# Kernel tuning notes

Measured on AMD Instinct MI355X. Metric: run time of the kernel, lower is better.

Reference implementation:

```python
import jax, jax.numpy as jnp
import numpy as np
from math import pi

B, L, S, D, H, M, DK, IND, KS = 8, 3072, 3072, 512, 8, 2, 64, 96, 25


def _linear(x, W, b):
    return x @ W + b


def _moving_avg(x, k):
    # Autoformer-style moving average with edge replication, stride 1.  x: [B, T, D]
    pad = (k - 1) // 2
    xp = jnp.concatenate([jnp.repeat(x[:, :1], pad, axis=1), x,
                          jnp.repeat(x[:, -1:], pad, axis=1)], axis=1)
    c = jnp.cumsum(xp, axis=1)
    c = jnp.concatenate([jnp.zeros_like(c[:, :1]), c], axis=1)
    return (c[:, k:] - c[:, :-k]) / k


def _trend_norm(x, g, b):
    # series_decomp(kernel=25): LayerNorm the seasonal part, add back the trend.
    trend = _moving_avg(x, KS)
    seas = x - trend
    mu = jnp.mean(seas, axis=-1, keepdims=True)
    var = jnp.var(seas, axis=-1, keepdims=True)
    return (seas - mu) * jax.lax.rsqrt(var + 1e-5) * g + b + trend


def _quat_attention(q, k, v, q_om, q_th, k_om, k_th):
    # q: [B,Lq,H,E]; k,v: [B,Sk,H,E]; omegas/thetas: [B,*,H,M]
    Bq, Lq, Hh, E = q.shape
    Sk = k.shape[1]
    Mm = q_om.shape[-1]
    qpos = (jnp.arange(Lq, dtype=q.dtype) / Lq)[None, :, None, None]
    kpos = (jnp.arange(Sk, dtype=q.dtype) / Sk)[None, :, None, None]
    Qa = q_om * qpos + q_th
    Ka = k_om * kpos + k_th
    Qc, Qs = jnp.cos(Qa), jnp.sin(Qa)
    Kc, Ks = jnp.cos(Ka), jnp.sin(Ka)
    q0, q1, q2, q3 = jnp.split(q, 4, axis=-1)
    k0, k1, k2, k3 = jnp.split(k, 4, axis=-1)
    op = lambda a, t: jnp.einsum('blhe,blhm->blhme', a, t)
    Qr = jnp.concatenate([op(q0, Qc) - op(q1, Qs), op(q1, Qc) + op(q0, Qs),
                          op(q2, Qc) + op(q3, Qs), op(q3, Qc) - op(q2, Qs)], axis=-1)
    Kr = jnp.concatenate([op(k0, Kc) - op(k2, Ks), op(k1, Kc) - op(k3, Ks),
                          op(k2, Kc) + op(k0, Ks), op(k3, Kc) + op(k1, Ks)], axis=-1)
    scores = jnp.einsum('blhme,bshme->bhls', Qr, Kr) / Mm
    scale = 1.0 / jnp.sqrt(jnp.asarray(E, q.dtype))
    A = jax.nn.softmax(scale * scores, axis=-1)
    return jnp.einsum('bhls,bshd->blhd', A, v)


def _ltr_layer(p, queries, keys, values):
    Bq, Lq, _ = queries.shape
    Sk = keys.shape[1]
    # kernel_size=1 convs == pointwise linears
    q_om = jax.nn.relu(_linear(queries, p['Wqo'], p['bqo'])).reshape(Bq, Lq, H, M)
    k_om = jax.nn.relu(_linear(keys, p['Wko'], p['bko'])).reshape(Bq, Sk, H, M)
    q_th = (jnp.tanh(_linear(queries, p['Wqt'], p['bqt'])) * pi).reshape(Bq, Lq, H, M)
    k_th = (jnp.tanh(_linear(keys, p['Wkt'], p['bkt'])) * pi).reshape(Bq, Sk, H, M)
    q = _linear(queries, p['Wq'], p['bq']).reshape(Bq, Lq, H, DK)
    k = _linear(keys, p['Wk'], p['bk']).reshape(Bq, Sk, H, DK)
    v = _linear(values, p['Wv'], p['bv']).reshape(Bq, Sk, H, DK)
    out = _quat_attention(q, k, v, q_om, q_th, k_om, k_th).reshape(Bq, Lq, H * DK)
    # D-matrix penalty == first-order difference along sequence
    om_pen = jnp.sum(jnp.diff(q_om, axis=1) ** 2) + jnp.sum(jnp.diff(k_om, axis=1) ** 2)
    th_pen = jnp.sum(q_th ** 2) + jnp.sum(k_th ** 2)
    return _linear(out, p['Wo'], p['bo']), om_pen, th_pen


def setup_inputs() -> dict:
    key = jax.random.key(0)
    ks = iter(jax.random.split(key, 32))
    rn = lambda shape, s=1.0: jax.random.normal(next(ks), shape, jnp.float32) * s
    w = 0.03  # ~1/sqrt(d_model)
    return dict(
        queries=rn((B, L, D)), keys=rn((B, S, D)), values=rn((B, S, D)),
        Wq=rn((2, D, D), w), bq=jnp.zeros((2, D), jnp.float32),
        Wk=rn((2, D, D), w), bk=jnp.zeros((2, D), jnp.float32),
        Wv=rn((2, D, D), w), bv=jnp.zeros((2, D), jnp.float32),
        Wqo=rn((2, D, M * H), w), bqo=jnp.zeros((2, M * H), jnp.float32),
        Wko=rn((2, D, M * H), w), bko=jnp.zeros((2, M * H), jnp.float32),
        Wqt=rn((2, D, M * H), w), bqt=jnp.zeros((2, M * H), jnp.float32),
        Wkt=rn((2, D, M * H), w), bkt=jnp.zeros((2, M * H), jnp.float32),
        Wo=rn((2, D, D), w), bo=jnp.zeros((2, D), jnp.float32),
        I=rn((1, IND, D), w),
        ln_g=jnp.ones((D,), jnp.float32), ln_b=jnp.zeros((D,), jnp.float32),
    )


def reference(queries, keys, values, Wq, bq, Wk, bk, Wv, bv, Wqo, bqo, Wko, bko,
              Wqt, bqt, Wkt, bkt, Wo, bo, I, ln_g, ln_b):
    def lp(i):
        return dict(Wq=Wq[i], bq=bq[i], Wk=Wk[i], bk=bk[i], Wv=Wv[i], bv=bv[i],
                    Wqo=Wqo[i], bqo=bqo[i], Wko=Wko[i], bko=bko[i],
                    Wqt=Wqt[i], bqt=bqt[i], Wkt=Wkt[i], bkt=bkt[i],
                    Wo=Wo[i], bo=bo[i])
    Bq = queries.shape[0]
    inducings = jnp.broadcast_to(I, (Bq, IND, D))
    inducings, om1, th1 = _ltr_layer(lp(0), inducings, keys, values)
    inducings = _trend_norm(inducings, ln_g, ln_b)
    out, om2, th2 = _ltr_layer(lp(1), queries, inducings, inducings)
    return out, om1 + om2, th1 + th2
```

## Files before the change

### kernel.cpp

```cpp
#include <hip/hip_runtime.h>
#include <math.h>

#define PI_F 3.14159265358979323846f

namespace {
constexpr int B_ = 8;
constexpr int L_ = 3072;
constexpr int S_ = 3072;
constexpr int H_ = 8;
constexpr int NF = 544;
constexpr int NSC = 8;
constexpr int SCHUNK = S_ / NSC;
}

typedef __attribute__((ext_vector_type(8))) short bf16x8;
typedef __attribute__((ext_vector_type(4))) float f32x4;

__device__ inline f32x4 mfma16(bf16x8 a, bf16x8 b, f32x4 c) {
  return __builtin_amdgcn_mfma_f32_16x16x32_bf16(a, b, c, 0, 0, 0);
}

__device__ inline ushort f2bf(float f) {
  union { float f; unsigned u; } v;
  v.f = f;
  unsigned r = v.u + 0x7FFFu + ((v.u >> 16) & 1u);
  return (ushort)(r >> 16);
}

__device__ inline void gl_lds16(const void* g, void* l) {
  __builtin_amdgcn_global_load_lds(
      (const __attribute__((address_space(1))) unsigned int*)g,
      (__attribute__((address_space(3))) unsigned int*)l, 16, 0, 0);
}

__device__ inline int xcd_swizzle(int flat, int nwg) {
  int q = nwg >> 3, r = nwg & 7;
  int xcd = flat & 7, ix = flat >> 3;
  return (xcd < r ? xcd * (q + 1) : r * (q + 1) + (xcd - r) * q) + ix;
}

__global__ void init_pen(float* pen) {
  if (threadIdx.x < 16) pen[threadIdx.x] = 0.f;
}

__global__ void write_pen(const float* __restrict__ pen, float* __restrict__ out) {
  if (threadIdx.x == 0) out[12582912] = pen[0];
  if (threadIdx.x == 1) out[12582913] = pen[1];
}

__global__ void pack_w(const float* __restrict__ Wm, const float* __restrict__ Wo_,
                       const float* __restrict__ Wt, const float* __restrict__ bm,
                       const float* __restrict__ bo_, const float* __restrict__ bt,
                       float* __restrict__ Wcat, float* __restrict__ bcat) {
  int gid = blockIdx.x * 256 + threadIdx.x;
  if (gid < 512 * 544) {
    int k = gid / 544, n = gid % 544;
    float v;
    if (n < 512) v = Wm[(size_t)k * 512 + n];
    else if (n < 528) v = Wo_[k * 16 + (n - 512)];
    else v = Wt[k * 16 + (n - 528)];
    Wcat[gid] = v;
  }
  if (gid < 544) {
    float v;
    if (gid < 512) v = bm[gid];
    else if (gid < 528) v = bo_[gid - 512];
    else v = bt[gid - 528];
    bcat[gid] = v;
  }
}

__global__ void pack_wt_fused(const float* __restrict__ Wm, const float* __restrict__ Wo_,
                              const float* __restrict__ Wt, const float* __restrict__ bm,
                              const float* __restrict__ bo_, const float* __restrict__ bt,
                              ushort* __restrict__ BT, float* __restrict__ bias) {
  int gid = blockIdx.x * 256 + threadIdx.x;
  if (gid < 640 * 512) {
    int n = gid >> 9, k = gid & 511;
    float v = 0.f;
    if (n < 512) v = Wm[(size_t)k * 512 + n];
    else if (n < 528) v = Wo_[k * 16 + (n - 512)];
    else if (n < 544) v = Wt[k * 16 + (n - 528)];
    BT[gid] = f2bf(v);
  }
  if (gid < 544)
    bias[gid] = (gid < 512) ? bm[gid] : (gid < 528 ? bo_[gid - 512] : bt[gid - 528]);
}

__global__ void pack_wt_plain(const float* __restrict__ W, const float* __restrict__ b,
                              ushort* __restrict__ BT, float* __restrict__ bias) {
  int gid = blockIdx.x * 256 + threadIdx.x;
  if (gid < 512 * 512) {
    int n = gid >> 9, k = gid & 511;
    BT[gid] = f2bf(W[(size_t)k * 512 + n]);
  }
  if (gid < 512) bias[gid] = b[gid];
}

__global__ __launch_bounds__(256)
void cast_bf16(const float* __restrict__ src, ushort* __restrict__ dst, int n8) {
  int gid = blockIdx.x * 256 + threadIdx.x;
  if (gid < n8) {
    float4 a = ((const float4*)src)[(size_t)gid * 2];
    float4 b = ((const float4*)src)[(size_t)gid * 2 + 1];
    ushort u[8] = {f2bf(a.x), f2bf(a.y), f2bf(a.z), f2bf(a.w),
                   f2bf(b.x), f2bf(b.y), f2bf(b.z), f2bf(b.w)};
    ((uint4*)dst)[gid] = *(uint4*)u;
  }
}

__global__ __launch_bounds__(256)
void gemm_bf16_mfma(const ushort* __restrict__ A, const ushort* __restrict__ BT,
                    const float* __restrict__ bias, void* __restrict__ Cv,
                    int ldc, int Nout, int act, int obf) {
  __shared__ ushort As[2][128][32];
  __shared__ ushort Bs[2][128][32];
  const int tid = threadIdx.x;
  const int wv = tid >> 6, lane = tid & 63, quad = lane >> 4, col = lane & 15;
  const int wm = wv & 1, wn = wv >> 1;

  const int nwg = gridDim.x * gridDim.y;
  const int flat = blockIdx.y * gridDim.x + blockIdx.x;
  const int nf = xcd_swizzle(flat, nwg);
  const int bx = nf % gridDim.x, by = nf / gridDim.x;
  const int m0 = by * 128, n0 = bx * 128;

  const int srow = lane >> 2;
  const int scol = (lane & 3) * 8;

  f32x4 acc[4][4];
#pragma unroll
  for (int i = 0; i < 4; ++i)
#pragma unroll
    for (int j = 0; j < 4; ++j) {
      f32x4 z = {0.f, 0.f, 0.f, 0.f};
      acc[i][j] = z;
    }

  const ushort* Ag = A + (size_t)(m0 + wv * 32) * 512;
  const ushort* Bg = BT + (size_t)(n0 + wv * 32) * 512;

  auto stage = [&](int bb, int k0) {
    gl_lds16(Ag + (size_t)srow * 512 + k0 + scol, &As[bb][wv * 32][0]);
    gl_lds16(Ag + (size_t)(srow + 16) * 512 + k0 + scol, &As[bb][wv * 32 + 16][0]);
    gl_lds16(Bg + (size_t)srow * 512 + k0 + scol, &Bs[bb][wv * 32][0]);
    gl_lds16(Bg + (size_t)(srow + 16) * 512 + k0 + scol, &Bs[bb][wv * 32 + 16][0]);
  };

  stage(0, 0);
  asm volatile("s_waitcnt vmcnt(0)" ::: "memory");
  __builtin_amdgcn_s_barrier();
  __builtin_amdgcn_sched_barrier(0);

  for (int i = 0; i < 16; ++i) {
    const int cur = i & 1;
    if (i < 15) stage(cur ^ 1, (i + 1) * 32);
    bf16x8 av[4], bv[4];
#pragma unroll
    for (int mi = 0; mi < 4; ++mi)
      av[mi] = *(const bf16x8*)&As[cur][wm * 64 + mi * 16 + col][quad * 8];
#pragma unroll
    for (int ni = 0; ni < 4; ++ni)
      bv[ni] = *(const bf16x8*)&Bs[cur][wn * 64 + ni * 16 + col][quad * 8];
#pragma unroll
    for (int mi = 0; mi < 4; ++mi)
#pragma unroll
      for (int ni = 0; ni < 4; ++ni)
        acc[mi][ni] = mfma16(av[mi], bv[ni], acc[mi][ni]);
    __builtin_amdgcn_sched_barrier(0);
    asm volatile("s_waitcnt vmcnt(0)" ::: "memory");
    __builtin_amdgcn_s_barrier();
    __builtin_amdgcn_sched_barrier(0);
  }

  float* Cf = (float*)Cv;
  ushort* Cu = (ushort*)Cv;
#pragma unroll
  for (int mi = 0; mi < 4; ++mi) {
#pragma unroll
    for (int ni = 0; ni < 4; ++ni) {
      int n = n0 + wn * 64 + ni * 16 + col;
      if (n >= Nout) continue;
      float bs = bias[n];
#pragma unroll
      for (int r = 0; r < 4; ++r) {
        int m = m0 + wm * 64 + mi * 16 + quad * 4 + r;
        float v = acc[mi][ni][r] + bs;
        if (act && n >= 512) v = (n < 528) ? fmaxf(v, 0.f) : tanhf(v) * PI_F;
        if (obf) Cu[(size_t)m * ldc + n] = f2bf(v);
        else Cf[(size_t)m * ldc + n] = v;
      }
    }
  }
}

__global__ __launch_bounds__(256)
void gemm_k512(const float* __restrict__ A, const float* __restrict__ W,
               const float* __restrict__ bias, float* __restrict__ C,
               int M, int N, int act) {
  __shared__ float As[16][68];
  __shared__ float Ws_[16][68];
  const int tid = threadIdx.x;
  const int tx = tid & 15, ty = tid >> 4;
  const int m0 = blockIdx.y * 64, n0 = blockIdx.x * 64;

  float acc[4][4];
#pragma unroll
  for (int i = 0; i < 4; ++i)
#pragma unroll
    for (int j = 0; j < 4; ++j) acc[i][j] = 0.f;

  const int arow = tid >> 2;
  const int acol4 = (tid & 3) * 4;
  const int wrow = tid >> 4;
  const int wcol4 = (tid & 15) * 4;

  for (int k0 = 0; k0 < 512; k0 += 16) {
    float4 av = make_float4(0.f, 0.f, 0.f, 0.f);
    int gm = m0 + arow;
    if (gm < M) av = *(const float4*)(A + (size_t)gm * 512 + k0 + acol4);
    As[acol4 + 0][arow] = av.x;
    As[acol4 + 1][arow] = av.y;
    As[acol4 + 2][arow] = av.z;
    As[acol4 + 3][arow] = av.w;
    float4 wv;
    int gn = n0 + wcol4;
    if (gn + 3 < N) {
      wv = *(const float4*)(W + (size_t)(k0 + wrow) * N + gn);
    } else {
      float tmp[4] = {0.f, 0.f, 0.f, 0.f};
      for (int u = 0; u < 4; ++u)
        if (gn + u < N) tmp[u] = W[(size_t)(k0 + wrow) * N + gn + u];
      wv = make_float4(tmp[0], tmp[1], tmp[2], tmp[3]);
    }
    *(float4*)&Ws_[wrow][wcol4] = wv;
    __syncthreads();
#pragma unroll
    for (int k = 0; k < 16; ++k) {
      float4 a4 = *(const float4*)&As[k][ty * 4];
      float4 b4 = *(const float4*)&Ws_[k][tx * 4];
      float a[4] = {a4.x, a4.y, a4.z, a4.w};
      float b[4] = {b4.x, b4.y, b4.z, b4.w};
#pragma unroll
      for (int i = 0; i < 4; ++i)
#pragma unroll
        for (int j = 0; j < 4; ++j) acc[i][j] = fmaf(a[i], b[j], acc[i][j]);
    }
    __syncthreads();
  }

#pragma unroll
  for (int i = 0; i < 4; ++i) {
    int gm = m0 + ty * 4 + i;
    if (gm >= M) continue;
#pragma unroll
    for (int j = 0; j < 4; ++j) {
      int gn = n0 + tx * 4 + j;
      if (gn >= N) continue;
      float v = acc[i][j] + bias[gn];
      if (act && gn >= 512) v = (gn < 528) ? fmaxf(v, 0.f) : tanhf(v) * PI_F;
      C[(size_t)gm * N + gn] = v;
    }
  }
}

__global__ __launch_bounds__(256)
void build_qr0(const float* __restrict__ QF0, ushort* __restrict__ Qr0bf) {
  const int l = blockIdx.x;
  const float* row = QF0 + (size_t)l * NF;
  __shared__ float2 trig[8][2];
  const int tid = threadIdx.x;
  if (tid < 16) {
    int h = tid >> 1, m = tid & 1;
    float om = row[512 + h * 2 + m], th = row[528 + h * 2 + m];
    float qa = fmaf(om, (float)l / 96.f, th);
    trig[h][m] = make_float2(cosf(qa), sinf(qa));
  }
  __syncthreads();
  for (int idx = tid; idx < 1024; idx += 256) {
    int h = idx >> 7, d = idx & 127;
    int m = d >> 6, r = d & 63, c = r >> 4, e = r & 15;
    float qc = row[h * 64 + c * 16 + e];
    float qp = row[h * 64 + (c ^ 1) * 16 + e];
    float2 tg = trig[h][m];
    float sgn = (c == 0 || c == 3) ? -1.f : 1.f;
    Qr0bf[((size_t)h * 96 + l) * 128 + d] = f2bf(fmaf(qc, tg.x, sgn * qp * tg.y));
  }
}

__global__ __launch_bounds__(256)
void build_kr0(const float* __restrict__ KF0, ushort* __restrict__ Kr0) {
  const int rs = blockIdx.x;
  const int b = rs / S_, s = rs - b * S_;
  const float* row = KF0 + (size_t)rs * NF;
  __shared__ float2 trig[8][2];
  const int tid = threadIdx.x;
  if (tid < 16) {
    int h = tid >> 1, m = tid & 1;
    float om = row[512 + h * 2 + m], th = row[528 + h * 2 + m];
    float ka = fmaf(om, (float)s * (1.f / (float)S_), th);
    trig[h][m] = make_float2(cosf(ka), sinf(ka));
  }
  __syncthreads();
  for (int idx = tid; idx < 512; idx += 256) {
    int h = idx >> 6, d = (idx & 63) * 2;
    int m = d >> 6, r = d & 63, c = r >> 4, e = r & 15;
    const float* rh = row + h * 64;
    float2 kc = *(const float2*)(rh + c * 16 + e);
    float2 kp = *(const float2*)(rh + (c ^ 2) * 16 + e);
    float2 tg = trig[h][m];
    float sgn = (c < 2) ? -1.f : 1.f;
    ushort2 u;
    u.x = f2bf(fmaf(kc.x, tg.x, sgn * kp.x * tg.y));
    u.y = f2bf(fmaf(kc.y, tg.x, sgn * kp.y * tg.y));
    *(ushort2*)&Kr0[(((size_t)(b * 8 + h)) * S_ + s) * 128 + d] = u;
  }
}

__global__ __launch_bounds__(256)
void build_vt0(const ushort* __restrict__ V0b, ushort* __restrict__ Vt0) {
  const int st = blockIdx.x, h = blockIdx.y, b = blockIdx.z;
  const int s0 = st * 64;
  const int tid = threadIdx.x;
  __shared__ ushort T[64][68];
  for (int idx = tid; idx < 4096; idx += 256) {
    int s = idx >> 6, d = idx & 63;
    T[d][s] = V0b[((size_t)(b * S_ + s0 + s)) * 512 + h * 64 + d];
  }
  __syncthreads();
  for (int idx = tid; idx < 2048; idx += 256) {
    int d = idx >> 5, s2 = (idx & 31) * 2;
    ushort2 u = *(const ushort2*)&T[d][s2];
    *(ushort2*)&Vt0[(((size_t)(b * 8 + h)) * 64 + d) * S_ + s0 + s2] = u;
  }
}

__global__ __launch_bounds__(256)
void build_kr1(const float* __restrict__ KF1, ushort* __restrict__ Kr1b) {
  const int rs = blockIdx.x;
  const int b = rs / 96, s = rs % 96;
  const float* row = KF1 + (size_t)rs * NF;
  __shared__ float2 trig[8][2];
  const int tid = threadIdx.x;
  if (tid < 16) {
    int h = tid >> 1, m = tid & 1;
    float om = row[512 + h * 2 + m], th = row[528 + h * 2 + m];
    float ka = fmaf(om, (float)s / 96.f, th);
    trig[h][m] = make_float2(cosf(ka), sinf(ka));
  }
  __syncthreads();
  for (int idx = tid; idx < 512; idx += 256) {
    int h = idx >> 6, d = (idx & 63) * 2;
    int m = d >> 6, r = d & 63, c = r >> 4, e = r & 15;
    const float* rh = row + h * 64;
    float2 kc = *(const float2*)(rh + c * 16 + e);
    float2 kp = *(const float2*)(rh + (c ^ 2) * 16 + e);
    float2 tg = trig[h][m];
    float sgn = (c < 2) ? -1.f : 1.f;
    ushort2 u;
    u.x = f2bf(fmaf(kc.x, tg.x, sgn * kp.x * tg.y));
    u.y = f2bf(fmaf(kc.y, tg.x, sgn * kp.y * tg.y));
    *(ushort2*)&Kr1b[(((size_t)(b * 8 + h)) * 96 + s) * 128 + d] = u;
  }
}

__global__ __launch_bounds__(256)
void build_qr1(const float* __restrict__ QF1, ushort* __restrict__ Qr1) {
  const int rl = blockIdx.x;
  const int b = rl / L_, l = rl - b * L_;
  const float* row = QF1 + (size_t)rl * NF;
  __shared__ float2 trig[8][2];
  const int tid = threadIdx.x;
  if (tid < 16) {
    int h = tid >> 1, m = tid & 1;
    float om = row[512 + h * 2 + m], th = row[528 + h * 2 + m];
    float qa = fmaf(om, (float)l * (1.f / (float)L_), th);
    trig[h][m] = make_float2(cosf(qa), sinf(qa));
  }
  __syncthreads();
  for (int idx = tid; idx < 512; idx += 256) {
    int h = idx >> 6, d = (idx & 63) * 2;
    int m = d >> 6, r = d & 63, c = r >> 4, e = r & 15;
    const float* rh = row + h * 64;
    float2 qc = *(const float2*)(rh + c * 16 + e);
    float2 qp = *(const float2*)(rh + (c ^ 1) * 16 + e);
    float2 tg = trig[h][m];
    float sgn = (c == 0 || c == 3) ? -1.f : 1.f;
    ushort2 u;
    u.x = f2bf(fmaf(qc.x, tg.x, sgn * qp.x * tg.y));
    u.y = f2bf(fmaf(qc.y, tg.x, sgn * qp.y * tg.y));
    *(ushort2*)&Qr1[(((size_t)(b * 8 + h)) * L_ + l) * 128 + d] = u;
  }
}

__global__ __launch_bounds__(256)
void build_vt1(const float* __restrict__ V1, ushort* __restrict__ Vt1) {
  const int h = blockIdx.x, b = blockIdx.y;
  const int tid = threadIdx.x;
  __shared__ ushort T[64][104];
  for (int idx = tid; idx < 96 * 64; idx += 256) {
    int s = idx >> 6, d = idx & 63;
    T[d][s] = f2bf(V1[(size_t)(b * 96 + s) * 512 + h * 64 + d]);
  }
  __syncthreads();
  for (int idx = tid; idx < 64 * 12; idx += 256) {
    int d = idx / 12, c8 = (idx % 12) * 8;
    *(uint4*)&Vt1[(((size_t)(b * 8 + h)) * 64 + d) * 96 + c8] = *(const uint4*)&T[d][c8];
  }
}

__global__ __launch_bounds__(256)
void attn0_mfma(const ushort* __restrict__ Kr0, const ushort* __restrict__ Vt0,
                const ushort* __restrict__ Qr0bf, float* __restrict__ accP,
                float* __restrict__ sumP) {
  const int sc = blockIdx.x, h = blockIdx.y, b = blockIdx.z;
  const int tid = threadIdx.x;
  const int wv = tid >> 6, lane = tid & 63, quad = lane >> 4, col = lane & 15;

  __shared__ __align__(16) ushort Qs[96][136];
  __shared__ __align__(16) ushort Ps[96][72];
  __shared__ float rowsum[96];

  const int s0g = sc * SCHUNK;
  const ushort* Kb = Kr0 + ((size_t)(b * 8 + h) * S_ + s0g) * 128;
  const ushort* Vb = Vt0 + ((size_t)(b * 8 + h)) * 64 * S_ + s0g;

  bf16x8 bk[6][4];
#pragma unroll
  for (int t = 0; t < 6; ++t) {
    const ushort* Kt = Kb + ((size_t)(t * 64 + wv * 16 + col)) * 128;
#pragma unroll
    for (int k = 0; k < 4; ++k) bk[t][k] = *(const bf16x8*)(Kt + k * 32 + quad * 8);
  }
  bf16x8 bv[6][2];
  {
    const ushort* Vt = Vb + ((size_t)(wv * 16 + col)) * S_;
#pragma unroll
    for (int t = 0; t < 6; ++t) {
      bv[t][0] = *(const bf16x8*)(Vt + t * 64 + quad * 8);
      bv[t][1] = *(const bf16x8*)(Vt + t * 64 + 32 + quad * 8);
    }
  }
  __builtin_amdgcn_sched_barrier(0);

  const ushort* Qg = Qr0bf + (size_t)h * 96 * 128;
  for (int idx = tid; idx < 96 * 16; idx += 256) {
    int l = idx >> 4, c8 = (idx & 15) * 8;
    *(uint4*)&Qs[l][c8] = *(const uint4*)(Qg + (size_t)l * 128 + c8);
  }
  if (tid < 96) rowsum[tid] = 0.f;

  f32x4 oacc[6];
#pragma unroll
  for (int i = 0; i < 6; ++i) {
    f32x4 z = {0.f, 0.f, 0.f, 0.f};
    oacc[i] = z;
  }

  __syncthreads();

#pragma unroll
  for (int t = 0; t < 6; ++t) {
    f32x4 sacc[6];
#pragma unroll
    for (int mt = 0; mt < 6; ++mt) {
      f32x4 z = {0.f, 0.f, 0.f, 0.f};
      sacc[mt] = z;
#pragma unroll
      for (int k = 0; k < 4; ++k) {
        bf16x8 a = *(const bf16x8*)&Qs[mt * 16 + col][k * 32 + quad * 8];
        sacc[mt] = mfma16(a, bk[t][k], sacc[mt]);
      }
    }
#pragma unroll
    for (int mt = 0; mt < 6; ++mt) {
      float pr[4];
#pragma unroll
      for (int r = 0; r < 4; ++r) {
        float p = __expf(sacc[mt][r] * 0.0625f);
        pr[r] = p;
        Ps[mt * 16 + quad * 4 + r][wv * 16 + col] = f2bf(p);
      }
#pragma unroll
      for (int r = 0; r < 4; ++r) {
#pragma unroll
        for (int off = 1; off < 16; off <<= 1) pr[r] += __shfl_xor(pr[r], off);
      }
      if (col == 0) {
#pragma unroll
        for (int r = 0; r < 4; ++r)
          atomicAdd(&rowsum[mt * 16 + quad * 4 + r], pr[r]);
      }
    }
    __syncthreads();
#pragma unroll
    for (int mt = 0; mt < 6; ++mt) {
      bf16x8 a0 = *(const bf16x8*)&Ps[mt * 16 + col][quad * 8];
      oacc[mt] = mfma16(a0, bv[t][0], oacc[mt]);
      bf16x8 a1 = *(const bf16x8*)&Ps[mt * 16 + col][32 + quad * 8];
      oacc[mt] = mfma16(a1, bv[t][1], oacc[mt]);
    }
    __syncthreads();
  }
  const size_t pbase = (((size_t)(b * 8 + h)) * NSC + sc) * 96;
#pragma unroll
  for (int mt = 0; mt < 6; ++mt) {
#pragma unroll
    for (int r = 0; r < 4; ++r) {
      int l = mt * 16 + quad * 4 + r;
      accP[(pbase + l) * 64 + wv * 16 + col] = oacc[mt][r];
    }
  }
  if (tid < 96) sumP[pbase + tid] = rowsum[tid];
}

__global__ __launch_bounds__(256)
void attn0_stage2(const float* __restrict__ accP, const float* __restrict__ sumP,
                  float* __restrict__ attn0) {
  const int l = blockIdx.x, b = blockIdx.y;
  const int tid = threadIdx.x;
  for (int e = tid; e < 512; e += 256) {
    int h = e >> 6, d = e & 63;
    size_t base = ((size_t)(b * 8 + h)) * NSC * 96;
    float num = 0.f, den = 0.f;
    for (int scv = 0; scv < NSC; ++scv) {
      size_t pb = base + (size_t)scv * 96 + l;
      num += accP[pb * 64 + d];
      den += sumP[pb];
    }
    attn0[((size_t)(b * 96 + l)) * 512 + e] = num / den;
  }
}

__global__ __launch_bounds__(256)
void trend_norm(const float* __restrict__ y, const float* __restrict__ g,
                const float* __restrict__ be, float* __restrict__ outp) {
  const int t = blockIdx.x, b = blockIdx.y;
  const int tid = threadIdx.x;
  __shared__ float red[256];
  __shared__ float red2[256];
  float seas[2], trend[2];
  float lsum = 0.f, lsum2 = 0.f;
#pragma unroll
  for (int u = 0; u < 2; ++u) {
    int d = tid + u * 256;
    float tr = 0.f;
    for (int j = -12; j <= 12; ++j) {
      int tt = t + j;
      tt = tt < 0 ? 0 : (tt > 95 ? 95 : tt);
      tr += y[((size_t)(b * 96 + tt)) * 512 + d];
    }
    tr *= (1.f / 25.f);
    float x = y[((size_t)(b * 96 + t)) * 512 + d];
    float se = x - tr;
    seas[u] = se;
    trend[u] = tr;
    lsum += se;
    lsum2 += se * se;
  }
  red[tid] = lsum;
  red2[tid] = lsum2;
  __syncthreads();
  for (int off = 128; off > 0; off >>= 1) {
    if (tid < off) {
      red[tid] += red[tid + off];
      red2[tid] += red2[tid + off];
    }
    __syncthreads();
  }
  float mu = red[0] / 512.f;
  float var = red2[0] / 512.f - mu * mu;
  float rs = rsqrtf(var + 1e-5f);
#pragma unroll
  for (int u = 0; u < 2; ++u) {
    int d = tid + u * 256;
    outp[((size_t)(b * 96 + t)) * 512 + d] = (seas[u] - mu) * rs * g[d] + be[d] + trend[u];
  }
}

__global__ __launch_bounds__(256)
void penalty(const float* __restrict__ base, int R, int nb, float mult,
             float* __restrict__ pen) {
  const int tid = threadIdx.x;
  size_t gid = (size_t)blockIdx.x * 256 + tid;
  size_t total = (size_t)nb * R * 16;
  float omv = 0.f, thv = 0.f;
  if (gid < total) {
    int j = (int)(gid & 15);
    size_t row = gid >> 4;
    int s = (int)(row % R);
    const float* r0 = base + row * NF;
    float th = r0[528 + j];
    thv = th * th;
    if (s < R - 1) {
      float d = r0[NF + 512 + j] - r0[512 + j];
      omv = d * d;
    }
  }
  __shared__ float ro[256], rt[256];
  ro[tid] = omv;
  rt[tid] = thv;
  __syncthreads();
  for (int off = 128; off > 0; off >>= 1) {
    if (tid < off) {
      ro[tid] += ro[tid + off];
      rt[tid] += rt[tid + off];
    }
    __syncthreads();
  }
  if (tid == 0) {
    atomicAdd(pen + 0, mult * ro[0]);
    atomicAdd(pen + 1, mult * rt[0]);
  }
}

__global__ __launch_bounds__(256)
void attn1_mfma(const ushort* __restrict__ Qr1, const ushort* __restrict__ Kr1b,
                const ushort* __restrict__ Vt1, ushort* __restrict__ attn1) {
  const int nwg = gridDim.x * gridDim.y * gridDim.z;
  const int flat = (blockIdx.z * gridDim.y + blockIdx.y) * gridDim.x + blockIdx.x;
  const int nf = xcd_swizzle(flat, nwg);
  const int lt = nf % gridDim.x;
  const int rest = nf / gridDim.x;
  const int h = rest % gridDim.y, b = rest / gridDim.y;
  const int l0 = lt * 64;
  const int tid = threadIdx.x;
  const int wv = tid >> 6, lane = tid & 63, quad = lane >> 4, col = lane & 15;

  __shared__ __align__(16) ushort Ks[96][136];
  __shared__ __align__(16) ushort Vs[64][104];
  __shared__ __align__(16) ushort Ps[64][104];
  ushort(*Os)[72] = reinterpret_cast<ushort(*)[72]>(&Ks[0][0]);

  const ushort* Qg = Qr1 + ((size_t)(b * 8 + h) * L_ + l0) * 128;
  const ushort* Kg = Kr1b + (size_t)(b * 8 + h) * 96 * 128;
  const ushort* Vg = Vt1 + (size_t)(b * 8 + h) * 64 * 96;

  for (int idx = tid; idx < 96 * 16; idx += 256) {
    int r = idx >> 4, c8 = (idx & 15) * 8;
    *(uint4*)&Ks[r][c8] = *(const uint4*)(Kg + (size_t)r * 128 + c8);
  }
  for (int idx = tid; idx < 64 * 12; idx += 256) {
    int r = idx / 12, c8 = (idx % 12) * 8;
    *(uint4*)&Vs[r][c8] = *(const uint4*)(Vg + (size_t)r * 96 + c8);
  }
  bf16x8 aq[4];
#pragma unroll
  for (int k = 0; k < 4; ++k)
    aq[k] = *(const bf16x8*)(Qg + ((size_t)(wv * 16 + col)) * 128 + k * 32 + quad * 8);
  __syncthreads();

  f32x4 sacc[6];
#pragma unroll
  for (int nt = 0; nt < 6; ++nt) {
    f32x4 z = {0.f, 0.f, 0.f, 0.f};
    sacc[nt] = z;
#pragma unroll
    for (int k = 0; k < 4; ++k) {
      bf16x8 bkf = *(const bf16x8*)&Ks[nt * 16 + col][k * 32 + quad * 8];
      sacc[nt] = mfma16(aq[k], bkf, sacc[nt]);
    }
  }
  float rsum[4] = {0.f, 0.f, 0.f, 0.f};
#pragma unroll
  for (int nt = 0; nt < 6; ++nt) {
#pragma unroll
    for (int r = 0; r < 4; ++r) {
      float p = __expf(sacc[nt][r] * 0.0625f);
      Ps[wv * 16 + quad * 4 + r][nt * 16 + col] = f2bf(p);
      rsum[r] += p;
    }
  }
#pragma unroll
  for (int r = 0; r < 4; ++r) {
#pragma unroll
    for (int off = 1; off < 16; off <<= 1) rsum[r] += __shfl_xor(rsum[r], off);
  }
  __syncthreads();
  bf16x8 ap[3];
#pragma unroll
  for (int kt = 0; kt < 3; ++kt)
    ap[kt] = *(const bf16x8*)&Ps[wv * 16 + col][kt * 32 + quad * 8];
  f32x4 oacc[4];
#pragma unroll
  for (int nt = 0; nt < 4; ++nt) {
    f32x4 z = {0.f, 0.f, 0.f, 0.f};
    oacc[nt] = z;
#pragma unroll
    for (int kt = 0; kt < 3; ++kt) {
      bf16x8 bvf = *(const bf16x8*)&Vs[nt * 16 + col][kt * 32 + quad * 8];
      oacc[nt] = mfma16(ap[kt], bvf, oacc[nt]);
    }
  }
  float inv[4];
#pragma unroll
  for (int r = 0; r < 4; ++r) inv[r] = 1.f / rsum[r];
#pragma unroll
  for (int nt = 0; nt < 4; ++nt) {
#pragma unroll
    for (int r = 0; r < 4; ++r) {
      Os[wv * 16 + quad * 4 + r][nt * 16 + col] = f2bf(oacc[nt][r] * inv[r]);
    }
  }
  __syncthreads();
  for (int idx = tid; idx < 64 * 8; idx += 256) {
    int l = idx >> 3, c8 = (idx & 7) * 8;
    *(uint4*)(attn1 + (size_t)(b * L_ + l0 + l) * 512 + h * 64 + c8) =
        *(const uint4*)&Os[l][c8];
  }
}

extern "C" void kernel_launch(void* const* d_in, const int* in_sizes, int n_in,
                              void* d_out, int out_size, void* d_ws, size_t ws_size,
                              hipStream_t stream) {
  (void)in_sizes; (void)n_in; (void)out_size; (void)ws_size;
  const float* queries = (const float*)d_in[0];
  const float* keys = (const float*)d_in[1];
  const float* values = (const float*)d_in[2];
  const float* Wq = (const float*)d_in[3];
  const float* bq = (const float*)d_in[4];
  const float* Wk = (const float*)d_in[5];
  const float* bk = (const float*)d_in[6];
  const float* Wv = (const float*)d_in[7];
  const float* bv = (const float*)d_in[8];
  const float* Wqo = (const float*)d_in[9];
  const float* bqo = (const float*)d_in[10];
  const float* Wko = (const float*)d_in[11];
  const float* bko = (const float*)d_in[12];
  const float* Wqt = (const float*)d_in[13];
  const float* bqt = (const float*)d_in[14];
  const float* Wkt = (const float*)d_in[15];
  const float* bkt = (const float*)d_in[16];
  const float* Wo = (const float*)d_in[17];
  const float* bo = (const float*)d_in[18];
  const float* I = (const float*)d_in[19];
  const float* ln_g = (const float*)d_in[20];
  const float* ln_b = (const float*)d_in[21];
  float* out = (float*)d_out;

  float* ws = (float*)d_ws;
  size_t off = 0;
  auto alloc = [&](size_t n) {
    float* p = ws + off;
    off += (n + 3) & ~(size_t)3;
    return p;
  };
  auto allocU = [&](size_t n) { return (ushort*)alloc((n + 1) / 2); };

  float* WCAT0Q = alloc(512 * 544);
  float* WCAT1K = alloc(512 * 544);
  float* BCAT0Q = alloc(544);
  float* BCAT1K = alloc(544);
  ushort* BT0K = allocU(640 * 512);
  ushort* BT1Q = allocU(640 * 512);
  ushort* BTV0 = allocU(512 * 512);
  ushort* BTO1 = allocU(512 * 512);
  float* B0K = alloc(544);
  float* B1Q = alloc(544);
  float* BV0 = alloc(512);
  float* BO1 = alloc(512);
  float* pen = alloc(16);
  float* QF0 = alloc(96 * 544);
  ushort* Qr0bf = allocU(8 * 96 * 128);
  float* KF0 = alloc((size_t)24576 * 544);
  float* V0 = alloc((size_t)24576 * 512);
  float* attn0 = alloc(768 * 512);
  float* y0 = alloc(768 * 512);
  float* xind = alloc(768 * 512);
  float* KF1 = alloc(768 * 544);
  float* V1 = alloc(768 * 512);
  ushort* Kr1b = allocU((size_t)64 * 96 * 128);
  ushort* Vt1 = allocU((size_t)64 * 64 * 96);
  float* accP = alloc((size_t)64 * NSC * 96 * 64);
  float* sumP = alloc((size_t)64 * NSC * 96);
  ushort* XB1 = allocU((size_t)24576 * 512);
  ushort* XB2 = allocU((size_t)24576 * 512);
  ushort* Kr0U = XB1;
  ushort* Vt0U = allocU((size_t)64 * 64 * S_);
  float* QF1 = KF0;
  ushort* V0b = (ushort*)V0;
  ushort* Qr1U = (ushort*)V0;

  init_pen<<<1, 64, 0, stream>>>(pen);
  const int packBlocks = (512 * 544 + 255) / 256;
  pack_w<<<packBlocks, 256, 0, stream>>>(Wq, Wqo, Wqt, bq, bqo, bqt, WCAT0Q, BCAT0Q);
  pack_w<<<packBlocks, 256, 0, stream>>>(Wk + 262144, Wko + 8192, Wkt + 8192,
                                         bk + 512, bko + 16, bkt + 16, WCAT1K, BCAT1K);
  pack_wt_fused<<<(640 * 512 + 255) / 256, 256, 0, stream>>>(
      Wk, Wko, Wkt, bk, bko, bkt, BT0K, B0K);
  pack_wt_fused<<<(640 * 512 + 255) / 256, 256, 0, stream>>>(
      Wq + 262144, Wqo + 8192, Wqt + 8192, bq + 512, bqo + 16, bqt + 16, BT1Q, B1Q);
  pack_wt_plain<<<(512 * 512 + 255) / 256, 256, 0, stream>>>(Wv, bv, BTV0, BV0);
  pack_wt_plain<<<(512 * 512 + 255) / 256, 256, 0, stream>>>(Wo + 262144, bo + 512,
                                                             BTO1, BO1);
  const int castBlocks = (24576 * 512 / 8 + 255) / 256;
  cast_bf16<<<castBlocks, 256, 0, stream>>>(keys, XB1, 24576 * 512 / 8);
  cast_bf16<<<castBlocks, 256, 0, stream>>>(values, XB2, 24576 * 512 / 8);

  gemm_bf16_mfma<<<dim3(5, 192), 256, 0, stream>>>(XB1, BT0K, B0K, KF0, 544, 544, 1, 0);
  gemm_bf16_mfma<<<dim3(4, 192), 256, 0, stream>>>(XB2, BTV0, BV0, V0b, 512, 512, 0, 1);
  gemm_k512<<<dim3(9, 2), 256, 0, stream>>>(I, WCAT0Q, BCAT0Q, QF0, 96, 544, 1);
  build_qr0<<<96, 256, 0, stream>>>(QF0, Qr0bf);
  penalty<<<(96 * 16 + 255) / 256, 256, 0, stream>>>(QF0, 96, 1, 8.f, pen);
  penalty<<<(24576 * 16 + 255) / 256, 256, 0, stream>>>(KF0, 3072, 8, 1.f, pen);
  build_kr0<<<24576, 256, 0, stream>>>(KF0, Kr0U);
  build_vt0<<<dim3(48, 8, 8), 256, 0, stream>>>(V0b, Vt0U);
  attn0_mfma<<<dim3(8, 8, 8), 256, 0, stream>>>(Kr0U, Vt0U, Qr0bf, accP, sumP);
  attn0_stage2<<<dim3(96, 8), 256, 0, stream>>>(accP, sumP, attn0);
  gemm_k512<<<dim3(8, 12), 256, 0, stream>>>(attn0, Wo, bo, y0, 768, 512, 0);
  trend_norm<<<dim3(96, 8), 256, 0, stream>>>(y0, ln_g, ln_b, xind);

  gemm_k512<<<dim3(9, 12), 256, 0, stream>>>(xind, WCAT1K, BCAT1K, KF1, 768, 544, 1);
  gemm_k512<<<dim3(8, 12), 256, 0, stream>>>(xind, Wv + 262144, bv + 512, V1, 768, 512, 0);
  build_kr1<<<768, 256, 0, stream>>>(KF1, Kr1b);
  build_vt1<<<dim3(8, 8), 256, 0, stream>>>(V1, Vt1);
  penalty<<<(768 * 16 + 255) / 256, 256, 0, stream>>>(KF1, 96, 8, 1.f, pen);
  cast_bf16<<<castBlocks, 256, 0, stream>>>(queries, XB1, 24576 * 512 / 8);
  gemm_bf16_mfma<<<dim3(5, 192), 256, 0, stream>>>(XB1, BT1Q, B1Q, QF1, 544, 544, 1, 0);
  penalty<<<(24576 * 16 + 255) / 256, 256, 0, stream>>>(QF1, 3072, 8, 1.f, pen);
  build_qr1<<<24576, 256, 0, stream>>>(QF1, Qr1U);
  attn1_mfma<<<dim3(48, 8, 8), 256, 0, stream>>>(Qr1U, Kr1b, Vt1, XB2);
  gemm_bf16_mfma<<<dim3(4, 192), 256, 0, stream>>>(XB2, BTO1, BO1, out, 512, 512, 0, 0);
  write_pen<<<1, 64, 0, stream>>>(pen, out);
}
```

Baseline: 794.7 us.

## Deepen GEMM LDS prefetch pipeline and stage attention K/V tiles through LDS

The GEMM main loop now issues the next two K-slices ahead and waits with a partial vmcnt, so global-to-LDS loads overlap with the MFMA work instead of draining every iteration. The first-layer attention kernel no longer preloads all K and V fragments into registers up front. It loads each 64-row K/V tile cooperatively into new LDS buffers per iteration, which lowers register pressure but adds LDS traffic and an extra barrier per tile.

```diff
diff --git a/kernel.cpp b/kernel.cpp
--- a/kernel.cpp
+++ b/kernel.cpp
@@ -148,13 +148,13 @@
   };
 
   stage(0, 0);
-  asm volatile("s_waitcnt vmcnt(0)" ::: "memory");
-  __builtin_amdgcn_s_barrier();
-  __builtin_amdgcn_sched_barrier(0);
+  stage(1, 32);
 
   for (int i = 0; i < 16; ++i) {
     const int cur = i & 1;
-    if (i < 15) stage(cur ^ 1, (i + 1) * 32);
+    if (i < 15) asm volatile("s_waitcnt vmcnt(4)" ::: "memory");
+    else        asm volatile("s_waitcnt vmcnt(0)" ::: "memory");
+    __builtin_amdgcn_s_barrier();
     bf16x8 av[4], bv[4];
 #pragma unroll
     for (int mi = 0; mi < 4; ++mi)
@@ -168,9 +168,8 @@
       for (int ni = 0; ni < 4; ++ni)
         acc[mi][ni] = mfma16(av[mi], bv[ni], acc[mi][ni]);
     __builtin_amdgcn_sched_barrier(0);
-    asm volatile("s_waitcnt vmcnt(0)" ::: "memory");
     __builtin_amdgcn_s_barrier();
-    __builtin_amdgcn_sched_barrier(0);
+    if (i < 14) stage(cur, (i + 2) * 32);
   }
 
   float* Cf = (float*)Cv;
@@ -418,30 +417,10 @@
   const int wv = tid >> 6, lane = tid & 63, quad = lane >> 4, col = lane & 15;
 
   __shared__ __align__(16) ushort Qs[96][136];
+  __shared__ __align__(16) ushort Ks[64][136];
+  __shared__ __align__(16) ushort Vt[64][72];
   __shared__ __align__(16) ushort Ps[96][72];
   __shared__ float rowsum[96];
-
-  const int s0g = sc * SCHUNK;
-  const ushort* Kb = Kr0 + ((size_t)(b * 8 + h) * S_ + s0g) * 128;
-  const ushort* Vb = Vt0 + ((size_t)(b * 8 + h)) * 64 * S_ + s0g;
-
-  bf16x8 bk[6][4];
-#pragma unroll
-  for (int t = 0; t < 6; ++t) {
-    const ushort* Kt = Kb + ((size_t)(t * 64 + wv * 16 + col)) * 128;
-#pragma unroll
-    for (int k = 0; k < 4; ++k) bk[t][k] = *(const bf16x8*)(Kt + k * 32 + quad * 8);
-  }
-  bf16x8 bv[6][2];
-  {
-    const ushort* Vt = Vb + ((size_t)(wv * 16 + col)) * S_;
-#pragma unroll
-    for (int t = 0; t < 6; ++t) {
-      bv[t][0] = *(const bf16x8*)(Vt + t * 64 + quad * 8);
-      bv[t][1] = *(const bf16x8*)(Vt + t * 64 + 32 + quad * 8);
-    }
-  }
-  __builtin_amdgcn_sched_barrier(0);
 
   const ushort* Qg = Qr0bf + (size_t)h * 96 * 128;
   for (int idx = tid; idx < 96 * 16; idx += 256) {
@@ -457,10 +436,25 @@
     oacc[i] = z;
   }
 
-  __syncthreads();
-
-#pragma unroll
+  const int s0g = sc * SCHUNK;
+  const ushort* Kb = Kr0 + ((size_t)(b * 8 + h) * S_ + s0g) * 128;
+  const ushort* Vb = Vt0 + ((size_t)(b * 8 + h)) * 64 * S_ + s0g;
+
   for (int t = 0; t < 6; ++t) {
+    __syncthreads();
+    for (int idx = tid; idx < 64 * 16; idx += 256) {
+      int s = idx >> 4, c8 = (idx & 15) * 8;
+      *(uint4*)&Ks[s][c8] = *(const uint4*)(Kb + ((size_t)(t * 64 + s)) * 128 + c8);
+    }
+    for (int idx = tid; idx < 64 * 8; idx += 256) {
+      int d = idx >> 3, c8 = (idx & 7) * 8;
+      *(uint4*)&Vt[d][c8] = *(const uint4*)(Vb + (size_t)d * S_ + t * 64 + c8);
+    }
+    __syncthreads();
+    bf16x8 bk[4];
+#pragma unroll
+    for (int k = 0; k < 4; ++k)
+      bk[k] = *(const bf16x8*)&Ks[wv * 16 + col][k * 32 + quad * 8];
     f32x4 sacc[6];
 #pragma unroll
     for (int mt = 0; mt < 6; ++mt) {
@@ -469,7 +463,7 @@
 #pragma unroll
       for (int k = 0; k < 4; ++k) {
         bf16x8 a = *(const bf16x8*)&Qs[mt * 16 + col][k * 32 + quad * 8];
-        sacc[mt] = mfma16(a, bk[t][k], sacc[mt]);
+        sacc[mt] = mfma16(a, bk[k], sacc[mt]);
       }
     }
 #pragma unroll
@@ -493,15 +487,17 @@
       }
     }
     __syncthreads();
+    bf16x8 bv0 = *(const bf16x8*)&Vt[wv * 16 + col][quad * 8];
+    bf16x8 bv1 = *(const bf16x8*)&Vt[wv * 16 + col][32 + quad * 8];
 #pragma unroll
     for (int mt = 0; mt < 6; ++mt) {
       bf16x8 a0 = *(const bf16x8*)&Ps[mt * 16 + col][quad * 8];
-      oacc[mt] = mfma16(a0, bv[t][0], oacc[mt]);
+      oacc[mt] = mfma16(a0, bv0, oacc[mt]);
       bf16x8 a1 = *(const bf16x8*)&Ps[mt * 16 + col][32 + quad * 8];
-      oacc[mt] = mfma16(a1, bv[t][1], oacc[mt]);
-    }
-    __syncthreads();
-  }
+      oacc[mt] = mfma16(a1, bv1, oacc[mt]);
+    }
+  }
+  __syncthreads();
   const size_t pbase = (((size_t)(b * 8 + h)) * NSC + sc) * 96;
 #pragma unroll
   for (int mt = 0; mt < 6; ++mt) {
```

New measurement: 770.4 us. 3.1% less time.
